# Performance work log

Hardware: AMD Instinct MI355X
Metric: run time of the kernel (lower is better)

The kernel has to match this reference:

```python
import jax, jax.numpy as jnp
import numpy as np
from math import factorial as fac

LMAX = 3
NMAX = 3
RC = 6.0
UNIT = RC / 3.0  # atomic_unit = rc/3
NSPEC = 4
N_ATOMS = 1000000


def _nnl():
    # a_{n,l} = 1 / ((2l+1) * 2^(2n+l) * n! * (n+l)!); nnl = sqrt(a_n a_n')
    a = np.array([[1.0 / ((2 * l + 1) * 2 ** (2 * n + l) * fac(n) * fac(n + l))
                   for l in range(LMAX + 1)] for n in range(NMAX + 1)])
    return jnp.asarray(np.sqrt(a[None] * a[:, None]), jnp.float32)  # (n, n', L+1)


def _yr_yi():
    one = np.ones((LMAX + 1, LMAX + 1))
    Yr = 2 * np.tril(one) - np.eye(LMAX + 1)   # real parts: diag weight 1 (m=0), lower weight 2
    Yi = 2 * np.triu(one, 1)                   # imag parts: strict upper weight 2
    return jnp.asarray(Yr, jnp.float32), jnp.asarray(Yi, jnp.float32)


def _sh_single(v):
    # Solid harmonics r^l * Ylm for one atom, packed into a (L+1, L+1) matrix:
    # Re(Y_l^m) at [l, l-m] (m=0 on the diagonal), Im(Y_l^m) at [l-m, l].
    x, y, z = v[0], v[1], v[2]
    r2 = x * x + y * y + z * z
    re = {(0, 0): jnp.asarray(0.28209479177387814, v.dtype)}  # 1/sqrt(4*pi)
    im = {(0, 0): jnp.zeros((), v.dtype)}
    for l in range(1, LMAX + 1):
        cl = -float(np.sqrt((2 * l + 1) / (2.0 * l)))
        re[(l, l)] = cl * (x * re[(l - 1, l - 1)] - y * im[(l - 1, l - 1)])
        im[(l, l)] = cl * (x * im[(l - 1, l - 1)] + y * re[(l - 1, l - 1)])
        g = float(np.sqrt(2 * l + 1))
        re[(l, l - 1)] = g * z * re[(l - 1, l - 1)]
        im[(l, l - 1)] = g * z * im[(l - 1, l - 1)]
        for m in range(l - 1):
            a = float(np.sqrt((4 * l * l - 1) / (l * l - m * m)))
            b = float(np.sqrt(((l - 1) ** 2 - m * m) / (4.0 * (l - 1) ** 2 - 1)))
            re[(l, m)] = a * (z * re[(l - 1, m)] - b * r2 * re[(l - 2, m)])
            im[(l, m)] = a * (z * im[(l - 1, m)] - b * r2 * im[(l - 2, m)])
    Y = jnp.zeros((LMAX + 1, LMAX + 1), v.dtype)
    for l in range(LMAX + 1):
        for m in range(l + 1):
            Y = Y.at[l, l - m].set(re[(l, m)])
            if m > 0:
                Y = Y.at[l - m, l].set(im[(l, m)])
    return Y


def _radial(dist):
    # Exp(-0.5 d^2/unit^2) * PolyCut(rc): smooth radial with polynomial cutoff
    cut = jnp.where(dist < RC, (1.0 - dist / RC) ** 2, 0.0)
    return jnp.exp(-0.5 * dist * dist / (UNIT * UNIT)) * cut


def _forward(coo, numbers):
    xyz = coo / UNIT
    d = jnp.sqrt(jnp.sum(xyz * xyz, axis=-1))              # (N,)
    n = 2.0 * jnp.arange(NMAX + 1, dtype=coo.dtype)        # exponents 2n
    r = _radial(UNIT * d)                                   # (N,)
    f = r[None] * d[None] ** n[:, None]                     # (nmax+1, N)
    Y = jnp.moveaxis(jax.vmap(_sh_single)(xyz), 0, -1)      # (L+1, L+1, N)
    onehot = (numbers[None, :] == jnp.arange(NSPEC)[:, None]).astype(coo.dtype)  # (S, N)
    # species-grouped reduction of the radial x Ylm outer product (fused einsum)
    c = jnp.einsum('kn,abn,sn->skab', f, Y, onehot)         # (S, nmax+1, L+1, L+1)
    Yr, Yi = _yr_yi()
    # p[a,b,n,m,l] = sum_m' Re-part + Im-part of c_{b,m} c*_{a,n} power spectrum
    p1 = jnp.einsum('bmlj,anlj,lj->abnml', c, c, Yr)
    p2 = jnp.einsum('bmil,anil,il->abnml', c, c, Yi)
    p = (p1 + p2) * _nnl()[None, None]
    return p.reshape(-1)                                    # dim = S^2 (nmax+1)^2 (L+1) = 1024


def setup_inputs() -> dict:
    key = jax.random.key(0)
    k1, k2 = jax.random.split(key)
    coo = 3.0 * jax.random.normal(k1, (N_ATOMS, 3), dtype=jnp.float32)
    numbers = jax.random.randint(k2, (N_ATOMS,), 0, NSPEC)
    return {"coo": coo, "numbers": numbers}


def reference(coo, numbers):
    return _forward(coo, numbers)
```

## Files before the change

kernel.cpp:

```cpp
#include <hip/hip_runtime.h>
#include <hip/hip_bf16.h>


typedef short short8 __attribute__((ext_vector_type(8)));
typedef float f32x4 __attribute__((ext_vector_type(4)));
typedef unsigned int uint4v __attribute__((ext_vector_type(4)));

#define NB 512

__global__ void __launch_bounds__(256) soap_accum(
    const float* __restrict__ coo, const int* __restrict__ numbers,
    int N, float* __restrict__ partials, float* __restrict__ c_ws,
    int* __restrict__ counter)
{
    __shared__ unsigned int lT[4][16][64];

    if (blockIdx.x == 0) {
        if (threadIdx.x < 256) c_ws[threadIdx.x] = 0.f;
        if (threadIdx.x == 0) *counter = 0;
    }

    const int lane = threadIdx.x & 63;
    const int w = threadIdx.x >> 6;
    const int g = lane >> 4;
    const int comp = lane & 15;

    unsigned int* lTw = &lT[w][0][0];

    const unsigned t4 = (unsigned)((comp & 7) << 2);
    const unsigned rb = (unsigned)(comp << 6);
    const uint4v* q0p = (const uint4v*)&lTw[rb + (( 8u * g)          ^ t4)];
    const uint4v* q1p = (const uint4v*)&lTw[rb + (( 8u * g + 4)      ^ t4)];
    const uint4v* q2p = (const uint4v*)&lTw[rb + ((32u + 8u * g)     ^ t4)];
    const uint4v* q3p = (const uint4v*)&lTw[rb + ((32u + 8u * g + 4) ^ t4)];

    f32x4 acc = {0.f, 0.f, 0.f, 0.f};

    const int stride = NB * 256;
    for (int base = (blockIdx.x * 4 + w) * 64; base < N; base += stride) {
        int i = base + lane;
        int ic = i < N ? i : N - 1;
        float x = coo[3 * ic + 0] * 0.5f;
        float y = coo[3 * ic + 1] * 0.5f;
        float z = coo[3 * ic + 2] * 0.5f;
        int num = numbers[ic];

        float r2 = x * x + y * y + z * z;
        float dq = sqrtf(r2);
        float tc = fmaxf(1.f - dq * (1.f / 3.f), 0.f);
        float r = __expf(-0.5f * r2) * (tc * tc);
        if (i >= N) r = 0.f;

        float fv[4];
        fv[0] = r; fv[1] = r * r2; fv[2] = fv[1] * r2; fv[3] = fv[2] * r2;

        const float Y00 = 0.28209479177387814f;
        float re11 = -0.34549414947133550f * x;
        float im11 = -0.34549414947133550f * y;
        float re10 =  0.48860251190291992f * z;
        float re22 = -1.11803398874989490f * (x * re11 - y * im11);
        float im22 = -1.11803398874989490f * (x * im11 + y * re11);
        float re21 =  2.23606797749978970f * z * re11;
        float im21 =  2.23606797749978970f * z * im11;
        float re20 =  1.93649167310370850f * (z * re10 - 0.16286750396763996f * r2);
        float re33 = -1.08012344973464350f * (x * re22 - y * im22);
        float im33 = -1.08012344973464350f * (x * im22 + y * re22);
        float re32 =  2.64575131106459070f * z * re22;
        float im32 =  2.64575131106459070f * z * im22;
        float re31 =  2.09165006633518890f * (z * re21 - 0.44721359549995793f * r2 * re11);
        float im31 =  2.09165006633518890f * (z * im21 - 0.44721359549995793f * r2 * im11);
        float re30 =  1.97202659436653870f * (z * re20 - 0.51639777949432220f * r2 * re10);

        float yv[16];
        yv[0] = Y00;  yv[1] = im11; yv[2]  = im22; yv[3]  = im33;
        yv[4] = re11; yv[5] = re10; yv[6]  = im21; yv[7]  = im32;
        yv[8] = re22; yv[9] = re21; yv[10] = re20; yv[11] = im31;
        yv[12] = re33; yv[13] = re32; yv[14] = re31; yv[15] = re30;

#pragma unroll
        for (int c = 0; c < 16; ++c) {
            float fsel = (num == (c >> 2)) ? fv[c & 3] : 0.f;
            unsigned d;
            asm("v_cvt_pk_bf16_f32 %0, %1, %2" : "=v"(d) : "v"(fsel), "v"(yv[c]));
            lTw[(c << 6) + (lane ^ ((c & 7) << 2))] = d;
        }

        uint4v q0 = *q0p, q1 = *q1p, q2 = *q2p, q3 = *q3p;

        short8 A0, B0, A1, B1;
#pragma unroll
        for (int e = 0; e < 4; ++e) {
            A0[e]     = (short)(q0[e] & 0xffffu);
            A0[4 + e] = (short)(q1[e] & 0xffffu);
            B0[e]     = (short)(q0[e] >> 16);
            B0[4 + e] = (short)(q1[e] >> 16);
            A1[e]     = (short)(q2[e] & 0xffffu);
            A1[4 + e] = (short)(q3[e] & 0xffffu);
            B1[e]     = (short)(q2[e] >> 16);
            B1[4 + e] = (short)(q3[e] >> 16);
        }

        acc = __builtin_amdgcn_mfma_f32_16x16x32_bf16(A0, B0, acc, 0, 0, 0);
        acc = __builtin_amdgcn_mfma_f32_16x16x32_bf16(A1, B1, acc, 0, 0, 0);
    }

    float* credw = (float*)&lT[w][0][0];
#pragma unroll
    for (int rr = 0; rr < 4; ++rr)
        credw[((lane >> 4) * 4 + rr) * 16 + (lane & 15)] = acc[rr];
    __syncthreads();

    int tt = threadIdx.x;
    partials[blockIdx.x * 256 + tt] =
        ((float*)&lT[0][0][0])[tt] + ((float*)&lT[1][0][0])[tt] +
        ((float*)&lT[2][0][0])[tt] + ((float*)&lT[3][0][0])[tt];
}

__global__ void __launch_bounds__(256) soap_reduce_final(
    const float* __restrict__ partials, float* __restrict__ c_ws,
    int* __restrict__ counter, float* __restrict__ out)
{
    __shared__ float cs[256];
    __shared__ int lastflag;
    int t = threadIdx.x;

    float v = 0.f;
    for (int r = blockIdx.x; r < NB; r += 32)
        v += partials[r * 256 + t];
    atomicAdd(&c_ws[t], v);
    __syncthreads();
    if (t == 0) {
        __threadfence();
        lastflag = (atomicAdd(counter, 1) == 31);
    }
    __syncthreads();
    if (!lastflag) return;

    __threadfence();
    cs[t] = __hip_atomic_load(&c_ws[t], __ATOMIC_RELAXED,
                              __HIP_MEMORY_SCOPE_AGENT);
    __syncthreads();

    const float fact[7] = {1.f, 1.f, 2.f, 6.f, 24.f, 120.f, 720.f};
#pragma unroll
    for (int k = 0; k < 4; ++k) {
        int o = k * 256 + t;
        int l = o & 3, m = (o >> 2) & 3, n = (o >> 4) & 3,
            b = (o >> 6) & 3, a = (o >> 8) & 3;
        const float* cbm = &cs[(b * 4 + m) * 16];
        const float* can = &cs[(a * 4 + n) * 16];
        float vv = 0.f;
        for (int j = 0; j <= l; ++j) {
            float wgt = (j == l) ? 1.f : 2.f;
            vv += wgt * cbm[l * 4 + j] * can[l * 4 + j];
        }
        for (int i = 0; i < l; ++i)
            vv += 2.f * cbm[i * 4 + l] * can[i * 4 + l];
        float an = 1.0f / ((float)(2 * l + 1) * (float)(1 << (2 * n + l)) * fact[n] * fact[n + l]);
        float am = 1.0f / ((float)(2 * l + 1) * (float)(1 << (2 * m + l)) * fact[m] * fact[m + l]);
        out[o] = vv * sqrtf(an * am);
    }
}

extern "C" void kernel_launch(void* const* d_in, const int* in_sizes, int n_in,
                              void* d_out, int out_size, void* d_ws, size_t ws_size,
                              hipStream_t stream)
{
    const float* coo = (const float*)d_in[0];
    const int* numbers = (const int*)d_in[1];
    int N = in_sizes[1];

    float* c_ws = (float*)d_ws;
    int* counter = (int*)((float*)d_ws + 256);
    float* partials = (float*)d_ws + 512;

    hipLaunchKernelGGL(soap_accum, dim3(NB), dim3(256), 0, stream,
                       coo, numbers, N, partials, c_ws, counter);
    hipLaunchKernelGGL(soap_reduce_final, dim3(32), dim3(256), 0, stream,
                       partials, c_ws, counter, (float*)d_out);
}
```

Baseline: 18.24 us.

## Process four atoms per lane with vectorized loads and larger LDS tiles

Each lane now handles four consecutive atoms, loading coordinates and species with float4/int4 vector loads. It writes 4-wide packed bf16 rows into a larger per-wave LDS tile and issues eight MFMAs per iteration instead of two. The block count is halved, so there are fewer partials to reduce. The aim is fewer memory instructions and less per-iteration overhead, at the cost of higher register pressure, four times the LDS use, and a tail case where N is not a multiple of 4 that is not handled.

```diff
diff --git a/kernel.cpp b/kernel.cpp
--- a/kernel.cpp
+++ b/kernel.cpp
@@ -6,14 +6,14 @@
 typedef float f32x4 __attribute__((ext_vector_type(4)));
 typedef unsigned int uint4v __attribute__((ext_vector_type(4)));
 
-#define NB 512
+#define NB 256
 
 __global__ void __launch_bounds__(256) soap_accum(
     const float* __restrict__ coo, const int* __restrict__ numbers,
     int N, float* __restrict__ partials, float* __restrict__ c_ws,
     int* __restrict__ counter)
 {
-    __shared__ unsigned int lT[4][16][64];
+    __shared__ unsigned int lT[4][16][256];
 
     if (blockIdx.x == 0) {
         if (threadIdx.x < 256) c_ws[threadIdx.x] = 0.f;
@@ -28,80 +28,88 @@
     unsigned int* lTw = &lT[w][0][0];
 
     const unsigned t4 = (unsigned)((comp & 7) << 2);
-    const unsigned rb = (unsigned)(comp << 6);
-    const uint4v* q0p = (const uint4v*)&lTw[rb + (( 8u * g)          ^ t4)];
-    const uint4v* q1p = (const uint4v*)&lTw[rb + (( 8u * g + 4)      ^ t4)];
-    const uint4v* q2p = (const uint4v*)&lTw[rb + ((32u + 8u * g)     ^ t4)];
-    const uint4v* q3p = (const uint4v*)&lTw[rb + ((32u + 8u * g + 4) ^ t4)];
+    const unsigned rb = (unsigned)(comp << 8);
 
     f32x4 acc = {0.f, 0.f, 0.f, 0.f};
 
-    const int stride = NB * 256;
-    for (int base = (blockIdx.x * 4 + w) * 64; base < N; base += stride) {
-        int i = base + lane;
-        int ic = i < N ? i : N - 1;
-        float x = coo[3 * ic + 0] * 0.5f;
-        float y = coo[3 * ic + 1] * 0.5f;
-        float z = coo[3 * ic + 2] * 0.5f;
-        int num = numbers[ic];
+    const int stride = NB * 1024;
+    for (int base = (blockIdx.x * 4 + w) * 256; base < N; base += stride) {
+        int ib = base + 4 * lane;
+        bool valid = ib < N;
+        int ic = valid ? ib : N - 4;
 
-        float r2 = x * x + y * y + z * z;
-        float dq = sqrtf(r2);
-        float tc = fmaxf(1.f - dq * (1.f / 3.f), 0.f);
-        float r = __expf(-0.5f * r2) * (tc * tc);
-        if (i >= N) r = 0.f;
+        const float4* cp = (const float4*)(coo + 3 * ic);
+        float4 cA = cp[0], cB = cp[1], cC = cp[2];
+        int4 nm4 = *(const int4*)(numbers + ic);
+        int nm[4];
+        nm[0] = valid ? nm4.x : -1; nm[1] = valid ? nm4.y : -1;
+        nm[2] = valid ? nm4.z : -1; nm[3] = valid ? nm4.w : -1;
+        float ax[4] = {cA.x, cA.w, cB.z, cC.y};
+        float ay[4] = {cA.y, cB.x, cB.w, cC.z};
+        float az[4] = {cA.z, cB.y, cC.x, cC.w};
 
-        float fv[4];
-        fv[0] = r; fv[1] = r * r2; fv[2] = fv[1] * r2; fv[3] = fv[2] * r2;
+        unsigned d[4][16];
+#pragma unroll
+        for (int j = 0; j < 4; ++j) {
+            float x = ax[j] * 0.5f, y = ay[j] * 0.5f, z = az[j] * 0.5f;
+            float r2 = x * x + y * y + z * z;
+            float dq = sqrtf(r2);
+            float tc = fmaxf(1.f - dq * (1.f / 3.f), 0.f);
+            float r = __expf(-0.5f * r2) * (tc * tc);
+            float fvv[4];
+            fvv[0] = r; fvv[1] = r * r2; fvv[2] = fvv[1] * r2; fvv[3] = fvv[2] * r2;
 
-        const float Y00 = 0.28209479177387814f;
-        float re11 = -0.34549414947133550f * x;
-        float im11 = -0.34549414947133550f * y;
-        float re10 =  0.48860251190291992f * z;
-        float re22 = -1.11803398874989490f * (x * re11 - y * im11);
-        float im22 = -1.11803398874989490f * (x * im11 + y * re11);
-        float re21 =  2.23606797749978970f * z * re11;
-        float im21 =  2.23606797749978970f * z * im11;
-        float re20 =  1.93649167310370850f * (z * re10 - 0.16286750396763996f * r2);
-        float re33 = -1.08012344973464350f * (x * re22 - y * im22);
-        float im33 = -1.08012344973464350f * (x * im22 + y * re22);
-        float re32 =  2.64575131106459070f * z * re22;
-        float im32 =  2.64575131106459070f * z * im22;
-        float re31 =  2.09165006633518890f * (z * re21 - 0.44721359549995793f * r2 * re11);
-        float im31 =  2.09165006633518890f * (z * im21 - 0.44721359549995793f * r2 * im11);
-        float re30 =  1.97202659436653870f * (z * re20 - 0.51639777949432220f * r2 * re10);
+            const float Y00 = 0.28209479177387814f;
+            float re11 = -0.34549414947133550f * x;
+            float im11 = -0.34549414947133550f * y;
+            float re10 =  0.48860251190291992f * z;
+            float re22 = -1.11803398874989490f * (x * re11 - y * im11);
+            float im22 = -1.11803398874989490f * (x * im11 + y * re11);
+            float re21 =  2.23606797749978970f * z * re11;
+            float im21 =  2.23606797749978970f * z * im11;
+            float re20 =  1.93649167310370850f * (z * re10 - 0.16286750396763996f * r2);
+            float re33 = -1.08012344973464350f * (x * re22 - y * im22);
+            float im33 = -1.08012344973464350f * (x * im22 + y * re22);
+            float re32 =  2.64575131106459070f * z * re22;
+            float im32 =  2.64575131106459070f * z * im22;
+            float re31 =  2.09165006633518890f * (z * re21 - 0.44721359549995793f * r2 * re11);
+            float im31 =  2.09165006633518890f * (z * im21 - 0.44721359549995793f * r2 * im11);
+            float re30 =  1.97202659436653870f * (z * re20 - 0.51639777949432220f * r2 * re10);
 
-        float yv[16];
-        yv[0] = Y00;  yv[1] = im11; yv[2]  = im22; yv[3]  = im33;
-        yv[4] = re11; yv[5] = re10; yv[6]  = im21; yv[7]  = im32;
-        yv[8] = re22; yv[9] = re21; yv[10] = re20; yv[11] = im31;
-        yv[12] = re33; yv[13] = re32; yv[14] = re31; yv[15] = re30;
+            float yvv[16];
+            yvv[0] = Y00;  yvv[1] = im11; yvv[2]  = im22; yvv[3]  = im33;
+            yvv[4] = re11; yvv[5] = re10; yvv[6]  = im21; yvv[7]  = im32;
+            yvv[8] = re22; yvv[9] = re21; yvv[10] = re20; yvv[11] = im31;
+            yvv[12] = re33; yvv[13] = re32; yvv[14] = re31; yvv[15] = re30;
+
+#pragma unroll
+            for (int c = 0; c < 16; ++c) {
+                float fsel = (nm[j] == (c >> 2)) ? fvv[c & 3] : 0.f;
+                asm("v_cvt_pk_bf16_f32 %0, %1, %2"
+                    : "=v"(d[j][c]) : "v"(fsel), "v"(yvv[c]));
+            }
+        }
 
 #pragma unroll
         for (int c = 0; c < 16; ++c) {
-            float fsel = (num == (c >> 2)) ? fv[c & 3] : 0.f;
-            unsigned d;
-            asm("v_cvt_pk_bf16_f32 %0, %1, %2" : "=v"(d) : "v"(fsel), "v"(yv[c]));
-            lTw[(c << 6) + (lane ^ ((c & 7) << 2))] = d;
+            uint4v vv = {d[0][c], d[1][c], d[2][c], d[3][c]};
+            *(uint4v*)&lTw[(c << 8) + ((4 * lane) ^ ((c & 7) << 2))] = vv;
         }
 
-        uint4v q0 = *q0p, q1 = *q1p, q2 = *q2p, q3 = *q3p;
-
-        short8 A0, B0, A1, B1;
 #pragma unroll
-        for (int e = 0; e < 4; ++e) {
-            A0[e]     = (short)(q0[e] & 0xffffu);
-            A0[4 + e] = (short)(q1[e] & 0xffffu);
-            B0[e]     = (short)(q0[e] >> 16);
-            B0[4 + e] = (short)(q1[e] >> 16);
-            A1[e]     = (short)(q2[e] & 0xffffu);
-            A1[4 + e] = (short)(q3[e] & 0xffffu);
-            B1[e]     = (short)(q2[e] >> 16);
-            B1[4 + e] = (short)(q3[e] >> 16);
+        for (int m = 0; m < 8; ++m) {
+            uint4v q0 = *(const uint4v*)&lTw[rb + 32 * m + (( 8u * g)      ^ t4)];
+            uint4v q1 = *(const uint4v*)&lTw[rb + 32 * m + (( 8u * g + 4)  ^ t4)];
+            short8 A, B;
+#pragma unroll
+            for (int e = 0; e < 4; ++e) {
+                A[e]     = (short)(q0[e] & 0xffffu);
+                A[4 + e] = (short)(q1[e] & 0xffffu);
+                B[e]     = (short)(q0[e] >> 16);
+                B[4 + e] = (short)(q1[e] >> 16);
+            }
+            acc = __builtin_amdgcn_mfma_f32_16x16x32_bf16(A, B, acc, 0, 0, 0);
         }
-
-        acc = __builtin_amdgcn_mfma_f32_16x16x32_bf16(A0, B0, acc, 0, 0, 0);
-        acc = __builtin_amdgcn_mfma_f32_16x16x32_bf16(A1, B1, acc, 0, 0, 0);
     }
 
     float* credw = (float*)&lT[w][0][0];
```

New measurement: 19.33 us. 6.0% more time.

## Pack two atoms per lane in fp16 and feed f16 MFMA directly

Applied to the files above, without the earlier changes.

Each lane now handles two atoms, computing spherical harmonics and radial terms with packed half2 arithmetic instead of fp32. The A and B operands go into separate LDS planes, so they can be loaded as ready-made half8 vectors and issued as four f16 MFMAs with no bf16 unpacking or shuffling. The aim is fewer VALU instructions per atom and to drop the conversion and repacking overhead. In exchange it uses fp16 precision for the harmonics and radial polynomial terms, which risks overflow or underflow and reduced accuracy, and it doubles LDS per wave.

```diff
diff --git a/kernel.cpp b/kernel.cpp
--- a/kernel.cpp
+++ b/kernel.cpp
@@ -1,10 +1,12 @@
 #include <hip/hip_runtime.h>
 #include <hip/hip_bf16.h>
+#include <hip/hip_fp16.h>
 
 
-typedef short short8 __attribute__((ext_vector_type(8)));
 typedef float f32x4 __attribute__((ext_vector_type(4)));
 typedef unsigned int uint4v __attribute__((ext_vector_type(4)));
+typedef _Float16 h2 __attribute__((ext_vector_type(2)));
+typedef _Float16 half8 __attribute__((ext_vector_type(8)));
 
 #define NB 512
 
@@ -13,7 +15,7 @@
     int N, float* __restrict__ partials, float* __restrict__ c_ws,
     int* __restrict__ counter)
 {
-    __shared__ unsigned int lT[4][16][64];
+    __shared__ unsigned int lT[4][2][16][64];
 
     if (blockIdx.x == 0) {
         if (threadIdx.x < 256) c_ws[threadIdx.x] = 0.f;
@@ -25,86 +27,96 @@
     const int g = lane >> 4;
     const int comp = lane & 15;
 
-    unsigned int* lTw = &lT[w][0][0];
+    unsigned int* lA = &lT[w][0][0][0];
+    unsigned int* lB = &lT[w][1][0][0];
 
-    const unsigned t4 = (unsigned)((comp & 7) << 2);
-    const unsigned rb = (unsigned)(comp << 6);
-    const uint4v* q0p = (const uint4v*)&lTw[rb + (( 8u * g)          ^ t4)];
-    const uint4v* q1p = (const uint4v*)&lTw[rb + (( 8u * g + 4)      ^ t4)];
-    const uint4v* q2p = (const uint4v*)&lTw[rb + ((32u + 8u * g)     ^ t4)];
-    const uint4v* q3p = (const uint4v*)&lTw[rb + ((32u + 8u * g + 4) ^ t4)];
+    const unsigned swz = (unsigned)((comp & 7) << 2);
+    const unsigned rbase = (unsigned)(comp << 6);
+    unsigned rd[4];
+#pragma unroll
+    for (int m = 0; m < 4; ++m)
+        rd[m] = rbase + ((unsigned)(16 * m + 4 * g) ^ swz);
 
     f32x4 acc = {0.f, 0.f, 0.f, 0.f};
 
-    const int stride = NB * 256;
-    for (int base = (blockIdx.x * 4 + w) * 64; base < N; base += stride) {
-        int i = base + lane;
-        int ic = i < N ? i : N - 1;
-        float x = coo[3 * ic + 0] * 0.5f;
-        float y = coo[3 * ic + 1] * 0.5f;
-        float z = coo[3 * ic + 2] * 0.5f;
-        int num = numbers[ic];
+    const int stride = NB * 512;
+    for (int base = (blockIdx.x * 4 + w) * 128; base < N; base += stride) {
+        int i0 = base + lane, i1 = base + 64 + lane;
+        int ic0 = i0 < N ? i0 : N - 1, ic1 = i1 < N ? i1 : N - 1;
+        float X0 = coo[3 * ic0], Y0_ = coo[3 * ic0 + 1], Z0 = coo[3 * ic0 + 2];
+        float X1 = coo[3 * ic1], Y1_ = coo[3 * ic1 + 1], Z1 = coo[3 * ic1 + 2];
+        int num0 = i0 < N ? numbers[ic0] : -1;
+        int num1 = i1 < N ? numbers[ic1] : -1;
 
-        float r2 = x * x + y * y + z * z;
-        float dq = sqrtf(r2);
-        float tc = fmaxf(1.f - dq * (1.f / 3.f), 0.f);
-        float r = __expf(-0.5f * r2) * (tc * tc);
-        if (i >= N) r = 0.f;
+        float x0 = X0 * 0.5f, y0 = Y0_ * 0.5f, z0 = Z0 * 0.5f;
+        float x1 = X1 * 0.5f, y1 = Y1_ * 0.5f, z1 = Z1 * 0.5f;
+        float r20 = x0 * x0 + y0 * y0 + z0 * z0;
+        float r21 = x1 * x1 + y1 * y1 + z1 * z1;
+        float t0 = fmaxf(1.f - sqrtf(r20) * (1.f / 3.f), 0.f);
+        float t1 = fmaxf(1.f - sqrtf(r21) * (1.f / 3.f), 0.f);
+        float f00 = __expf(-0.5f * r20) * t0 * t0;
+        float f01 = __expf(-0.5f * r21) * t1 * t1;
 
-        float fv[4];
-        fv[0] = r; fv[1] = r * r2; fv[2] = fv[1] * r2; fv[3] = fv[2] * r2;
+        h2 fpk[4];
+        fpk[0] = (h2){(_Float16)f00, (_Float16)f01};
+        fpk[1] = (h2){(_Float16)(f00 * r20), (_Float16)(f01 * r21)};
+        fpk[2] = (h2){(_Float16)(f00 * r20 * r20), (_Float16)(f01 * r21 * r21)};
+        fpk[3] = (h2){(_Float16)(f00 * r20 * r20 * r20), (_Float16)(f01 * r21 * r21 * r21)};
 
-        const float Y00 = 0.28209479177387814f;
-        float re11 = -0.34549414947133550f * x;
-        float im11 = -0.34549414947133550f * y;
-        float re10 =  0.48860251190291992f * z;
-        float re22 = -1.11803398874989490f * (x * re11 - y * im11);
-        float im22 = -1.11803398874989490f * (x * im11 + y * re11);
-        float re21 =  2.23606797749978970f * z * re11;
-        float im21 =  2.23606797749978970f * z * im11;
-        float re20 =  1.93649167310370850f * (z * re10 - 0.16286750396763996f * r2);
-        float re33 = -1.08012344973464350f * (x * re22 - y * im22);
-        float im33 = -1.08012344973464350f * (x * im22 + y * re22);
-        float re32 =  2.64575131106459070f * z * re22;
-        float im32 =  2.64575131106459070f * z * im22;
-        float re31 =  2.09165006633518890f * (z * re21 - 0.44721359549995793f * r2 * re11);
-        float im31 =  2.09165006633518890f * (z * im21 - 0.44721359549995793f * r2 * im11);
-        float re30 =  1.97202659436653870f * (z * re20 - 0.51639777949432220f * r2 * re10);
+        h2 msk[4];
+#pragma unroll
+        for (int s = 0; s < 4; ++s)
+            msk[s] = (h2){(_Float16)(num0 == s ? 1.f : 0.f),
+                          (_Float16)(num1 == s ? 1.f : 0.f)};
 
-        float yv[16];
-        yv[0] = Y00;  yv[1] = im11; yv[2]  = im22; yv[3]  = im33;
-        yv[4] = re11; yv[5] = re10; yv[6]  = im21; yv[7]  = im32;
-        yv[8] = re22; yv[9] = re21; yv[10] = re20; yv[11] = im31;
-        yv[12] = re33; yv[13] = re32; yv[14] = re31; yv[15] = re30;
+        h2 xp = (h2){(_Float16)x0, (_Float16)x1};
+        h2 yp = (h2){(_Float16)y0, (_Float16)y1};
+        h2 zp = (h2){(_Float16)z0, (_Float16)z1};
+        h2 rp = (h2){(_Float16)r20, (_Float16)r21};
+
+        h2 re11 = (_Float16)-0.34549414947133550f * xp;
+        h2 im11 = (_Float16)-0.34549414947133550f * yp;
+        h2 re10 = (_Float16) 0.48860251190291992f * zp;
+        h2 re22 = (_Float16)-1.11803398874989490f * (xp * re11 - yp * im11);
+        h2 im22 = (_Float16)-1.11803398874989490f * (xp * im11 + yp * re11);
+        h2 re21 = (_Float16) 2.23606797749978970f * (zp * re11);
+        h2 im21 = (_Float16) 2.23606797749978970f * (zp * im11);
+        h2 re20 = (_Float16) 1.93649167310370850f * (zp * re10 - (_Float16)0.16286750396763996f * rp);
+        h2 re33 = (_Float16)-1.08012344973464350f * (xp * re22 - yp * im22);
+        h2 im33 = (_Float16)-1.08012344973464350f * (xp * im22 + yp * re22);
+        h2 re32 = (_Float16) 2.64575131106459070f * (zp * re22);
+        h2 im32 = (_Float16) 2.64575131106459070f * (zp * im22);
+        h2 re31 = (_Float16) 2.09165006633518890f * (zp * re21 - (_Float16)0.44721359549995793f * (rp * re11));
+        h2 im31 = (_Float16) 2.09165006633518890f * (zp * im21 - (_Float16)0.44721359549995793f * (rp * im11));
+        h2 re30 = (_Float16) 1.97202659436653870f * (zp * re20 - (_Float16)0.51639777949432220f * (rp * re10));
+
+        h2 ypk[16];
+        ypk[0] = (h2){(_Float16)0.28209479177387814f, (_Float16)0.28209479177387814f};
+        ypk[1] = im11; ypk[2]  = im22; ypk[3]  = im33;
+        ypk[4] = re11; ypk[5]  = re10; ypk[6]  = im21; ypk[7]  = im32;
+        ypk[8] = re22; ypk[9]  = re21; ypk[10] = re20; ypk[11] = im31;
+        ypk[12] = re33; ypk[13] = re32; ypk[14] = re31; ypk[15] = re30;
 
 #pragma unroll
         for (int c = 0; c < 16; ++c) {
-            float fsel = (num == (c >> 2)) ? fv[c & 3] : 0.f;
-            unsigned d;
-            asm("v_cvt_pk_bf16_f32 %0, %1, %2" : "=v"(d) : "v"(fsel), "v"(yv[c]));
-            lTw[(c << 6) + (lane ^ ((c & 7) << 2))] = d;
+            h2 fs = fpk[c & 3] * msk[c >> 2];
+            union { h2 h; unsigned u; } ua, ub;
+            ua.h = fs; ub.h = ypk[c];
+            unsigned idx = (unsigned)(c << 6) + ((unsigned)lane ^ ((unsigned)(c & 7) << 2));
+            lA[idx] = ua.u;
+            lB[idx] = ub.u;
         }
 
-        uint4v q0 = *q0p, q1 = *q1p, q2 = *q2p, q3 = *q3p;
-
-        short8 A0, B0, A1, B1;
 #pragma unroll
-        for (int e = 0; e < 4; ++e) {
-            A0[e]     = (short)(q0[e] & 0xffffu);
-            A0[4 + e] = (short)(q1[e] & 0xffffu);
-            B0[e]     = (short)(q0[e] >> 16);
-            B0[4 + e] = (short)(q1[e] >> 16);
-            A1[e]     = (short)(q2[e] & 0xffffu);
-            A1[4 + e] = (short)(q3[e] & 0xffffu);
-            B1[e]     = (short)(q2[e] >> 16);
-            B1[4 + e] = (short)(q3[e] >> 16);
+        for (int m = 0; m < 4; ++m) {
+            union { uint4v q; half8 h; } A, B;
+            A.q = *(const uint4v*)&lA[rd[m]];
+            B.q = *(const uint4v*)&lB[rd[m]];
+            acc = __builtin_amdgcn_mfma_f32_16x16x32_f16(A.h, B.h, acc, 0, 0, 0);
         }
-
-        acc = __builtin_amdgcn_mfma_f32_16x16x32_bf16(A0, B0, acc, 0, 0, 0);
-        acc = __builtin_amdgcn_mfma_f32_16x16x32_bf16(A1, B1, acc, 0, 0, 0);
     }
 
-    float* credw = (float*)&lT[w][0][0];
+    float* credw = (float*)&lT[w][0][0][0];
 #pragma unroll
     for (int rr = 0; rr < 4; ++rr)
         credw[((lane >> 4) * 4 + rr) * 16 + (lane & 15)] = acc[rr];
@@ -112,8 +124,8 @@
 
     int tt = threadIdx.x;
     partials[blockIdx.x * 256 + tt] =
-        ((float*)&lT[0][0][0])[tt] + ((float*)&lT[1][0][0])[tt] +
-        ((float*)&lT[2][0][0])[tt] + ((float*)&lT[3][0][0])[tt];
+        ((float*)&lT[0][0][0][0])[tt] + ((float*)&lT[1][0][0][0])[tt] +
+        ((float*)&lT[2][0][0][0])[tt] + ((float*)&lT[3][0][0][0])[tt];
 }
 
 __global__ void __launch_bounds__(256) soap_reduce_final(
```

Measured after the change: 17.69 us. 3.1% less time.
